# Kernel optimization log

Measured on AMD Instinct MI355X. Metric: run time of the kernel, lower is better.

Reference implementation:

```python
import jax, jax.numpy as jnp
import numpy as np

VOCAB, EMBED, HIDDEN, POL = 32000, 300, 1024, 3
BS, SEQ = 64, 512


def setup_inputs() -> dict:
    key = jax.random.key(0)
    ks = jax.random.split(key, 17)
    stdv = 1.0 / np.sqrt(HIDDEN)
    u = lambda k, shape: jax.random.uniform(k, shape, jnp.float32, -stdv, stdv)
    return {
        "text": jax.random.randint(ks[0], (BS, SEQ), 0, VOCAB),
        "embed_table": jax.random.normal(ks[1], (VOCAB, EMBED), jnp.float32),
        "U_i": u(ks[2], (EMBED, HIDDEN)), "U_f": u(ks[3], (EMBED, HIDDEN)),
        "U_c": u(ks[4], (EMBED, HIDDEN)), "U_o": u(ks[5], (EMBED, HIDDEN)),
        "V_i": u(ks[6], (HIDDEN, HIDDEN)), "V_f": u(ks[7], (HIDDEN, HIDDEN)),
        "V_c": u(ks[8], (HIDDEN, HIDDEN)), "V_o": u(ks[9], (HIDDEN, HIDDEN)),
        "b_i": u(ks[10], (HIDDEN,)), "b_f": u(ks[11], (HIDDEN,)),
        "b_c": u(ks[12], (HIDDEN,)), "b_o": u(ks[13], (HIDDEN,)),
        "W_dense": u(ks[14], (HIDDEN, POL)),
        "b_dense": u(ks[15], (POL,)),
    }


def _lstm_final_h(x, U_i, U_f, U_c, U_o, V_i, V_f, V_c, V_o, b_i, b_f, b_c, b_o):
    # x: [B, S, E]. Precompute all input projections once (big fused GEMM),
    # leaving only the recurrent h @ V matmuls inside the scan.
    bs = x.shape[0]
    H = V_i.shape[0]
    U = jnp.concatenate([U_i, U_f, U_c, U_o], axis=1)          # [E, 4H]
    b = jnp.concatenate([b_i, b_f, b_c, b_o], axis=0)          # [4H]
    xU = jnp.einsum('bse,eh->sbh', x, U) + b                   # [S, B, 4H]
    V = jnp.concatenate([V_i, V_f, V_c, V_o], axis=1)          # [H, 4H]

    def step(carry, xu_t):
        h, c = carry
        gates = xu_t + h @ V                                   # [B, 4H]
        xi, xf, xg, xo = jnp.split(gates, 4, axis=-1)
        i = jax.nn.sigmoid(xi)
        f = jax.nn.sigmoid(xf)
        g = jnp.tanh(xg)
        o = jax.nn.sigmoid(xo)
        c = f * c + i * g
        h = o * jnp.tanh(c)
        return (h, c), None

    h0 = jnp.zeros((bs, H), x.dtype)
    c0 = jnp.zeros((bs, H), x.dtype)
    (h_n, c_n), _ = jax.lax.scan(step, (h0, c0), xU)
    return h_n


def reference(text, embed_table, U_i, U_f, U_c, U_o, V_i, V_f, V_c, V_o,
              b_i, b_f, b_c, b_o, W_dense, b_dense):
    x = embed_table[text]                                      # [B, S, E]
    h_n = _lstm_final_h(x, U_i, U_f, U_c, U_o, V_i, V_f, V_c, V_o,
                        b_i, b_f, b_c, b_o)                    # [B, H]
    return h_n @ W_dense + b_dense                             # [B, POL]
```

## Files before the change

kernel.cpp:

```cpp
#include <hip/hip_runtime.h>
#include <stdint.h>

#define SEQL 512
#define BATCH 64
#define EMB 300
#define EMBP 320
#define HID 1024
#define NWG 64
#define UNITS 16
#define NCH 42
#define FSTR 16

typedef __attribute__((ext_vector_type(8))) short short8;
typedef __attribute__((ext_vector_type(4))) float f32x4;
typedef __attribute__((ext_vector_type(2))) unsigned int uint2v;

union Frag { short8 v; ushort u[8]; uint uu[4]; };
struct AF { uint2v lo, hi; };

__device__ __forceinline__ ushort f2bf(float f){
  union { float f; uint u; } c; c.f = f;
  return (ushort)((c.u + 0x7fffu + ((c.u >> 16) & 1u)) >> 16);
}

struct Params {
  const ushort* xbf;
  ushort* hbuf;
  float*  hfinal;
  int*    flags;
  ushort* wpack;
  const float* V[4];
  const float* U[4];
  const float* bia[4];
  const float* Wd;
  const float* bd;
  float* out;
};

__global__ void __launch_bounds__(256) prep(const int* __restrict__ text,
                                            const float* __restrict__ tab,
                                            ushort* __restrict__ xbf,
                                            ushort* __restrict__ hbuf,
                                            int* __restrict__ flags){
  const int tid = blockIdx.x * blockDim.x + threadIdx.x;
  const int nth = gridDim.x * blockDim.x;
  uint* hz = (uint*)hbuf;
  for (int i = tid; i < NWG*64*16/2; i += nth) hz[i] = 0u;
  if (tid < NWG*FSTR) flags[tid] = 0;
  const int nch = SEQL*BATCH*(EMBP/8);
  for (int ch = tid; ch < nch; ch += nth){
    const int e8 = ch % (EMBP/8);
    const int sb = ch / (EMBP/8);
    const int b  = sb & (BATCH-1);
    const int s  = sb >> 6;
    const int tok = text[b*SEQL + s];
    union { ushort u[8]; uint4 v; } o;
    #pragma unroll
    for (int j = 0; j < 8; j++){
      const int e = e8*8 + j;
      o.u[j] = f2bf(e < EMB ? tab[(size_t)tok*EMB + e] : 0.f);
    }
    *(uint4*)&xbf[(size_t)sb*EMBP + e8*8] = o.v;
  }
}

__global__ void __launch_bounds__(256) packw(Params p){
  const int bid  = blockIdx.x;
  const int w    = bid / NCH;
  const int kc   = bid % NCH;
  const int tid  = threadIdx.x;
  const int nt   = tid >> 6;
  const int lane = tid & 63;
  const int l4   = (lane >> 4) & 3;
  const int colg = w*UNITS + (lane & 15);
  Frag fr;
  #pragma unroll
  for (int j = 0; j < 8; j++){
    const int koff = ((j >> 2) << 4) + l4*4 + (j & 3);
    float v = 0.f;
    if (kc < 32){
      v = p.V[nt][(size_t)(kc*32 + koff)*HID + colg];
    } else {
      const int krow = (kc-32)*32 + koff;
      if (krow < EMB) v = p.U[nt][(size_t)krow*HID + colg];
    }
    fr.u[j] = f2bf(v);
  }
  *(short8*)&p.wpack[(((size_t)(w*NCH + kc)*4 + nt)*64 + lane)*8] = fr.v;
}

#define WISSUE(c) { \
    const ushort* wp_ = wpk + (size_t)(wave + 4*(c))*2048 + lane*8; \
    asm volatile("global_load_dwordx4 %0, %4, off\n\t" \
                 "global_load_dwordx4 %1, %4, off offset:1024\n\t" \
                 "global_load_dwordx4 %2, %4, off offset:2048\n\t" \
                 "global_load_dwordx4 %3, %4, off offset:3072" \
                 : "=&v"(wfr[(c)&3][0]), "=&v"(wfr[(c)&3][1]), \
                   "=&v"(wfr[(c)&3][2]), "=&v"(wfr[(c)&3][3]) \
                 : "v"(wp_) : "memory"); }

#define VISSUE(c) { \
    const ushort* bp_ = hcur + (size_t)(wave + 4*(c))*2048 + qk; \
    _Pragma("unroll") \
    for (int m_ = 0; m_ < 4; m_++){ \
      const ushort* rp_ = bp_ + (m_*16 + mrow)*16; \
      asm volatile("global_load_dwordx2 %0, %2, off sc0 sc1\n\t" \
                   "global_load_dwordx2 %1, %2, off offset:2048 sc0 sc1" \
                   : "=&v"(afr[(c)&3][m_].lo), "=&v"(afr[(c)&3][m_].hi) \
                   : "v"(rp_) : "memory"); \
    } }

#define VWAIT(n) { asm volatile("s_waitcnt vmcnt(" #n ")" ::: "memory"); \
                   __builtin_amdgcn_sched_barrier(0); }

#define VMFMA(c) { \
    _Pragma("unroll") \
    for (int m_ = 0; m_ < 4; m_++){ \
      Frag a_; \
      a_.uu[0] = afr[(c)&3][m_].lo[0]; a_.uu[1] = afr[(c)&3][m_].lo[1]; \
      a_.uu[2] = afr[(c)&3][m_].hi[0]; a_.uu[3] = afr[(c)&3][m_].hi[1]; \
      _Pragma("unroll") \
      for (int nt_ = 0; nt_ < 4; nt_++) \
        acc[m_][nt_] = __builtin_amdgcn_mfma_f32_16x16x32_bf16(a_.v, wfr[(c)&3][nt_], acc[m_][nt_], 0, 0, 0); \
    } }

__global__ void __launch_bounds__(256, 1) lstm_scan(Params p){
  __shared__ float buffer[2][64][68];
  __shared__ float cst[UNITS][BATCH];
  __shared__ float bias_l[64];

  const int w    = blockIdx.x;
  const int tid  = threadIdx.x;
  const int wave = tid >> 6;
  const int lane = tid & 63;
  const int n0   = w * UNITS;
  const int mrow = lane & 15;
  const int qk   = ((lane >> 4) & 3) << 2;
  const int nU   = (wave < 2) ? 3 : 2;
  const ushort* __restrict__ wpk = p.wpack + (size_t)w*NCH*2048;

  const int pl   = lane & 15;
  const int* fp  = p.flags + (2*(wave + 4*(pl >> 1)) + (pl & 1)) * FSTR;

  if (tid < 64) bias_l[tid] = p.bia[tid >> 4][n0 + (tid & 15)];
  for (int i = tid; i < UNITS*BATCH; i += 256) (&cst[0][0])[i] = 0.f;
  __syncthreads();

  for (int t = 0; t < SEQL; t++){
    const ushort* __restrict__ xt = p.xbf + (size_t)t * (BATCH*EMBP);

    f32x4 acc[4][4];
    #pragma unroll
    for (int m = 0; m < 4; m++)
      #pragma unroll
      for (int nt = 0; nt < 4; nt++)
        acc[m][nt] = (f32x4){0.f, 0.f, 0.f, 0.f};

    #pragma unroll
    for (int j3 = 0; j3 < 3; j3++){
      if (j3 < nU){
        const int kb  = (wave + 4*j3)*32;
        const int kcg = 32 + wave + 4*j3;
        Frag af[4];
        #pragma unroll
        for (int m = 0; m < 4; m++){
          const ushort* rp = xt + (size_t)(m*16 + mrow)*EMBP + kb + qk;
          uint2 lo = *(const uint2*)rp;
          uint2 hi = *(const uint2*)(rp + 16);
          af[m].uu[0] = lo.x; af[m].uu[1] = lo.y;
          af[m].uu[2] = hi.x; af[m].uu[3] = hi.y;
        }
        short8 wu[4];
        #pragma unroll
        for (int nt = 0; nt < 4; nt++)
          wu[nt] = *(const short8*)&wpk[(size_t)kcg*2048 + nt*512 + lane*8];
        #pragma unroll
        for (int m = 0; m < 4; m++)
          #pragma unroll
          for (int nt = 0; nt < 4; nt++)
            acc[m][nt] = __builtin_amdgcn_mfma_f32_16x16x32_bf16(af[m].v, wu[nt], acc[m][nt], 0, 0, 0);
      }
    }

    if (t > 0){
      for (;;){
        int v;
        asm volatile("global_load_dword %0, %1, off sc0 sc1\n\t"
                     "s_waitcnt vmcnt(0)"
                     : "=&v"(v) : "v"(fp) : "memory");
        if (__all(v >= t)) break;
        __builtin_amdgcn_s_sleep(1);
      }
      __builtin_amdgcn_sched_barrier(0);

      const ushort* __restrict__ hcur = p.hbuf + (size_t)(t & 1) * (NWG*64*16);
      AF afr[4][4];
      short8 wfr[4][4];
      VWAIT(0)
      WISSUE(0) VISSUE(0) WISSUE(1) VISSUE(1)
      WISSUE(2) VISSUE(2) WISSUE(3) VISSUE(3)
      VWAIT(36) VMFMA(0) WISSUE(4) VISSUE(4)
      VWAIT(36) VMFMA(1) WISSUE(5) VISSUE(5)
      VWAIT(36) VMFMA(2) WISSUE(6) VISSUE(6)
      VWAIT(36) VMFMA(3) WISSUE(7) VISSUE(7)
      VWAIT(36) VMFMA(4)
      VWAIT(24) VMFMA(5)
      VWAIT(12) VMFMA(6)
      VWAIT(0)  VMFMA(7)
    }

    const int fq = (lane >> 4) << 2;
    if (wave >= 2){
      #pragma unroll
      for (int m = 0; m < 4; m++)
        #pragma unroll
        for (int nt = 0; nt < 4; nt++)
          *(f32x4*)&buffer[wave-2][nt*16 + mrow][m*16 + fq] = acc[m][nt];
    }
    __syncthreads();
    if (wave < 2){
      #pragma unroll
      for (int m = 0; m < 4; m++)
        #pragma unroll
        for (int nt = 0; nt < 4; nt++){
          f32x4 o = *(f32x4*)&buffer[wave][nt*16 + mrow][m*16 + fq];
          o += acc[m][nt];
          *(f32x4*)&buffer[wave][nt*16 + mrow][m*16 + fq] = o;
        }
    }
    __syncthreads();

    const int eb = tid & 63;
    const int uq = tid >> 6;
    ushort* __restrict__ hnxt = p.hbuf + (size_t)((t+1) & 1) * (NWG*64*16);
    ushort hout[4]; float hfv[4];
    #pragma unroll
    for (int rr = 0; rr < 4; rr++){
      const int u = uq*4 + rr;
      float g0 = buffer[0][ 0+u][eb] + buffer[1][ 0+u][eb] + bias_l[ 0+u];
      float g1 = buffer[0][16+u][eb] + buffer[1][16+u][eb] + bias_l[16+u];
      float g2 = buffer[0][32+u][eb] + buffer[1][32+u][eb] + bias_l[32+u];
      float g3 = buffer[0][48+u][eb] + buffer[1][48+u][eb] + bias_l[48+u];
      float ig = 1.f/(1.f + __expf(-g0));
      float fg = 1.f/(1.f + __expf(-g1));
      float gg = 2.f/(1.f + __expf(-2.f*g2)) - 1.f;
      float og = 1.f/(1.f + __expf(-g3));
      float cv = fg * cst[u][eb] + ig * gg;
      cst[u][eb] = cv;
      float hv = og * (2.f/(1.f + __expf(-2.f*cv)) - 1.f);
      hout[rr] = f2bf(hv);
      hfv[rr] = hv;
    }
    {
      union { ushort u[4]; uint2v v; } pk;
      pk.u[0]=hout[0]; pk.u[1]=hout[1]; pk.u[2]=hout[2]; pk.u[3]=hout[3];
      ushort* sa = &hnxt[(size_t)w*1024 + eb*16 + uq*4];
      asm volatile("global_store_dwordx2 %0, %1, off sc0 sc1"
                   :: "v"(sa), "v"(pk.v) : "memory");
      if (t == SEQL-1){
        f32x4 fv; fv[0]=hfv[0]; fv[1]=hfv[1]; fv[2]=hfv[2]; fv[3]=hfv[3];
        float* fa = &p.hfinal[(size_t)eb*HID + n0 + uq*4];
        asm volatile("global_store_dwordx4 %0, %1, off sc0 sc1"
                     :: "v"(fa), "v"(fv) : "memory");
      }
    }
    asm volatile("s_waitcnt vmcnt(0)" ::: "memory");
    __syncthreads();
    if (tid == 0){
      int tv = t + 1;
      asm volatile("global_store_dword %0, %1, off sc0 sc1"
                   :: "v"(p.flags + w*FSTR), "v"(tv) : "memory");
    }
  }

  if (wave == 0){
    const int* ffp = p.flags + lane*FSTR;
    for (;;){
      int v;
      asm volatile("global_load_dword %0, %1, off sc0 sc1\n\t"
                   "s_waitcnt vmcnt(0)"
                   : "=&v"(v) : "v"(ffp) : "memory");
      if (__all(v >= SEQL)) break;
      __builtin_amdgcn_s_sleep(1);
    }
  }
  __syncthreads();

  float s0 = 0.f, s1 = 0.f, s2 = 0.f;
  {
    const float* ap = p.hfinal + (size_t)w * HID + tid;
    float h0, h1, h2, h3;
    asm volatile("global_load_dword %0, %4, off sc0 sc1\n\t"
                 "global_load_dword %1, %4, off offset:1024 sc0 sc1\n\t"
                 "global_load_dword %2, %4, off offset:2048 sc0 sc1\n\t"
                 "global_load_dword %3, %4, off offset:3072 sc0 sc1\n\t"
                 "s_waitcnt vmcnt(0)"
                 : "=&v"(h0), "=&v"(h1), "=&v"(h2), "=&v"(h3)
                 : "v"(ap) : "memory");
    const float hvv[4] = {h0, h1, h2, h3};
    #pragma unroll
    for (int j = 0; j < 4; j++){
      const int k = tid + 256*j;
      s0 = fmaf(hvv[j], p.Wd[k*3+0], s0);
      s1 = fmaf(hvv[j], p.Wd[k*3+1], s1);
      s2 = fmaf(hvv[j], p.Wd[k*3+2], s2);
    }
  }
  float* red = &buffer[0][0][0];
  red[tid*3+0] = s0; red[tid*3+1] = s1; red[tid*3+2] = s2;
  __syncthreads();
  for (int off = 128; off > 0; off >>= 1){
    if (tid < off){
      red[tid*3+0] += red[(tid+off)*3+0];
      red[tid*3+1] += red[(tid+off)*3+1];
      red[tid*3+2] += red[(tid+off)*3+2];
    }
    __syncthreads();
  }
  if (tid < 3) p.out[w*3 + tid] = red[tid] + p.bd[tid];
}

extern "C" void kernel_launch(void* const* d_in, const int* in_sizes, int n_in,
                              void* d_out, int out_size, void* d_ws, size_t ws_size,
                              hipStream_t stream){
  const int*   text = (const int*)d_in[0];
  const float* tab  = (const float*)d_in[1];

  Params p;
  char* ws = (char*)d_ws;
  size_t off = 0;
  p.xbf    = (const ushort*)(ws + off); off += (size_t)SEQL*BATCH*EMBP*2;
  p.hbuf   = (ushort*)(ws + off);       off += (size_t)2*NWG*64*16*2;
  p.hfinal = (float*)(ws + off);        off += (size_t)BATCH*HID*4;
  p.flags  = (int*)(ws + off);          off += (size_t)NWG*FSTR*4;
  p.wpack  = (ushort*)(ws + off);       off += (size_t)NWG*NCH*4*64*8*2;

  for (int g = 0; g < 4; g++){
    p.U[g]   = (const float*)d_in[2+g];
    p.V[g]   = (const float*)d_in[6+g];
    p.bia[g] = (const float*)d_in[10+g];
  }
  p.Wd  = (const float*)d_in[14];
  p.bd  = (const float*)d_in[15];
  p.out = (float*)d_out;

  prep<<<1024, 256, 0, stream>>>(text, tab, (ushort*)p.xbf, (ushort*)p.hbuf, p.flags);
  packw<<<NWG*NCH, 256, 0, stream>>>(p);
  lstm_scan<<<NWG, 256, 0, stream>>>(p);
}
```

Before: 4.167 ms.

## Halve persistent workgroups to 32 with 512 threads and gate-split waves

The persistent LSTM scan moves from 64 workgroups of 256 threads with 16 hidden units each to 32 workgroups of 512 threads with 32 units each. Each wave now owns one gate and half of the K range, and the waves are reduced through shared memory. The weight pack layout, h buffer layout, flag polling and final dense reduction are rewritten to match, and the recurrent load pipeline is deepened to 5 stages. The aim is fewer cross-workgroup flag syncs per step and more per-workgroup work to hide latency, at the cost of heavier per-workgroup weight streaming and fewer CUs in use.

```diff
diff --git a/kernel.cpp b/kernel.cpp
--- a/kernel.cpp
+++ b/kernel.cpp
@@ -6,8 +6,8 @@
 #define EMB 300
 #define EMBP 320
 #define HID 1024
-#define NWG 64
-#define UNITS 16
+#define NWG 32
+#define UNITS 32
 #define NCH 42
 #define FSTR 16
 
@@ -45,7 +45,7 @@
   const int tid = blockIdx.x * blockDim.x + threadIdx.x;
   const int nth = gridDim.x * blockDim.x;
   uint* hz = (uint*)hbuf;
-  for (int i = tid; i < NWG*64*16/2; i += nth) hz[i] = 0u;
+  for (int i = tid; i < NWG*64*UNITS/2; i += nth) hz[i] = 0u;
   if (tid < NWG*FSTR) flags[tid] = 0;
   const int nch = SEQL*BATCH*(EMBP/8);
   for (int ch = tid; ch < nch; ch += nth){
@@ -65,48 +65,50 @@
 }
 
 __global__ void __launch_bounds__(256) packw(Params p){
-  const int bid  = blockIdx.x;
-  const int w    = bid / NCH;
-  const int kc   = bid % NCH;
-  const int tid  = threadIdx.x;
-  const int nt   = tid >> 6;
-  const int lane = tid & 63;
-  const int l4   = (lane >> 4) & 3;
-  const int colg = w*UNITS + (lane & 15);
-  Frag fr;
+  const int bid = blockIdx.x;
+  const int w   = bid / NCH;
+  const int kc  = bid % NCH;
+  const int tid = threadIdx.x;
   #pragma unroll
-  for (int j = 0; j < 8; j++){
-    const int koff = ((j >> 2) << 4) + l4*4 + (j & 3);
-    float v = 0.f;
-    if (kc < 32){
-      v = p.V[nt][(size_t)(kc*32 + koff)*HID + colg];
-    } else {
-      const int krow = (kc-32)*32 + koff;
-      if (krow < EMB) v = p.U[nt][(size_t)krow*HID + colg];
-    }
-    fr.u[j] = f2bf(v);
-  }
-  *(short8*)&p.wpack[(((size_t)(w*NCH + kc)*4 + nt)*64 + lane)*8] = fr.v;
+  for (int r = 0; r < 2; r++){
+    const int item = tid + 256*r;
+    const int g    = item >> 7;
+    const int nt   = (item >> 6) & 1;
+    const int lane = item & 63;
+    const int l4   = (lane >> 4) & 3;
+    const int colg = w*UNITS + nt*16 + (lane & 15);
+    Frag fr;
+    #pragma unroll
+    for (int j = 0; j < 8; j++){
+      const int koff = ((j >> 2) << 4) + l4*4 + (j & 3);
+      float v = 0.f;
+      if (kc < 32){
+        v = p.V[g][(size_t)(kc*32 + koff)*HID + colg];
+      } else {
+        const int krow = (kc-32)*32 + koff;
+        if (krow < EMB) v = p.U[g][(size_t)krow*HID + colg];
+      }
+      fr.u[j] = f2bf(v);
+    }
+    *(short8*)&p.wpack[((((size_t)(w*NCH + kc)*4 + g)*2 + nt)*64 + lane)*8] = fr.v;
+  }
 }
 
 #define WISSUE(c) { \
-    const ushort* wp_ = wpk + (size_t)(wave + 4*(c))*2048 + lane*8; \
-    asm volatile("global_load_dwordx4 %0, %4, off\n\t" \
-                 "global_load_dwordx4 %1, %4, off offset:1024\n\t" \
-                 "global_load_dwordx4 %2, %4, off offset:2048\n\t" \
-                 "global_load_dwordx4 %3, %4, off offset:3072" \
-                 : "=&v"(wfr[(c)&3][0]), "=&v"(wfr[(c)&3][1]), \
-                   "=&v"(wfr[(c)&3][2]), "=&v"(wfr[(c)&3][3]) \
+    const ushort* wp_ = wpk + ((size_t)(kh2*16 + (c))*8 + g*2)*512 + lane*8; \
+    asm volatile("global_load_dwordx4 %0, %2, off\n\t" \
+                 "global_load_dwordx4 %1, %2, off offset:1024" \
+                 : "=&v"(wfr[(c)%5][0]), "=&v"(wfr[(c)%5][1]) \
                  : "v"(wp_) : "memory"); }
 
 #define VISSUE(c) { \
-    const ushort* bp_ = hcur + (size_t)(wave + 4*(c))*2048 + qk; \
+    const ushort* bp_ = hcur + (size_t)(kh2*16 + (c))*2048 + qk; \
     _Pragma("unroll") \
     for (int m_ = 0; m_ < 4; m_++){ \
-      const ushort* rp_ = bp_ + (m_*16 + mrow)*16; \
+      const ushort* rp_ = bp_ + (m_*16 + mrow)*32; \
       asm volatile("global_load_dwordx2 %0, %2, off sc0 sc1\n\t" \
-                   "global_load_dwordx2 %1, %2, off offset:2048 sc0 sc1" \
-                   : "=&v"(afr[(c)&3][m_].lo), "=&v"(afr[(c)&3][m_].hi) \
+                   "global_load_dwordx2 %1, %2, off offset:32 sc0 sc1" \
+                   : "=&v"(afr[(c)%5][m_].lo), "=&v"(afr[(c)%5][m_].hi) \
                    : "v"(rp_) : "memory"); \
     } }
 
@@ -117,68 +119,65 @@
     _Pragma("unroll") \
     for (int m_ = 0; m_ < 4; m_++){ \
       Frag a_; \
-      a_.uu[0] = afr[(c)&3][m_].lo[0]; a_.uu[1] = afr[(c)&3][m_].lo[1]; \
-      a_.uu[2] = afr[(c)&3][m_].hi[0]; a_.uu[3] = afr[(c)&3][m_].hi[1]; \
-      _Pragma("unroll") \
-      for (int nt_ = 0; nt_ < 4; nt_++) \
-        acc[m_][nt_] = __builtin_amdgcn_mfma_f32_16x16x32_bf16(a_.v, wfr[(c)&3][nt_], acc[m_][nt_], 0, 0, 0); \
+      a_.uu[0] = afr[(c)%5][m_].lo[0]; a_.uu[1] = afr[(c)%5][m_].lo[1]; \
+      a_.uu[2] = afr[(c)%5][m_].hi[0]; a_.uu[3] = afr[(c)%5][m_].hi[1]; \
+      acc[m_][0] = __builtin_amdgcn_mfma_f32_16x16x32_bf16(a_.v, wfr[(c)%5][0], acc[m_][0], 0, 0, 0); \
+      acc[m_][1] = __builtin_amdgcn_mfma_f32_16x16x32_bf16(a_.v, wfr[(c)%5][1], acc[m_][1], 0, 0, 0); \
     } }
 
-__global__ void __launch_bounds__(256, 1) lstm_scan(Params p){
-  __shared__ float buffer[2][64][68];
+#define STEP5(c) { VWAIT(40) VMFMA(c) WISSUE((c)+5) VISSUE((c)+5) }
+
+__global__ void __launch_bounds__(512, 1) lstm_scan(Params p){
+  __shared__ float buffer[4][UNITS][66];
   __shared__ float cst[UNITS][BATCH];
-  __shared__ float bias_l[64];
+  __shared__ float bias_l[4*UNITS];
 
   const int w    = blockIdx.x;
   const int tid  = threadIdx.x;
   const int wave = tid >> 6;
+  const int g    = wave & 3;
+  const int kh2  = wave >> 2;
   const int lane = tid & 63;
   const int n0   = w * UNITS;
   const int mrow = lane & 15;
   const int qk   = ((lane >> 4) & 3) << 2;
-  const int nU   = (wave < 2) ? 3 : 2;
-  const ushort* __restrict__ wpk = p.wpack + (size_t)w*NCH*2048;
+  const int fq   = (lane >> 4) << 2;
+  const ushort* __restrict__ wpk = p.wpack + (size_t)w*NCH*4096;
 
   const int pl   = lane & 15;
-  const int* fp  = p.flags + (2*(wave + 4*(pl >> 1)) + (pl & 1)) * FSTR;
-
-  if (tid < 64) bias_l[tid] = p.bia[tid >> 4][n0 + (tid & 15)];
-  for (int i = tid; i < UNITS*BATCH; i += 256) (&cst[0][0])[i] = 0.f;
+  const int* fp  = p.flags + (kh2*16 + pl) * FSTR;
+
+  if (tid < 4*UNITS) bias_l[tid] = p.bia[tid >> 5][n0 + (tid & 31)];
+  for (int i = tid; i < UNITS*BATCH; i += 512) (&cst[0][0])[i] = 0.f;
   __syncthreads();
 
   for (int t = 0; t < SEQL; t++){
     const ushort* __restrict__ xt = p.xbf + (size_t)t * (BATCH*EMBP);
 
-    f32x4 acc[4][4];
-    #pragma unroll
-    for (int m = 0; m < 4; m++)
+    f32x4 acc[4][2];
+    #pragma unroll
+    for (int m = 0; m < 4; m++){ acc[m][0] = (f32x4){0,0,0,0}; acc[m][1] = (f32x4){0,0,0,0}; }
+
+    #pragma unroll
+    for (int uc = 0; uc < 5; uc++){
+      const int ug  = kh2*5 + uc;
+      const int kb  = ug*32;
+      const int kcg = 32 + ug;
+      Frag af[4];
       #pragma unroll
-      for (int nt = 0; nt < 4; nt++)
-        acc[m][nt] = (f32x4){0.f, 0.f, 0.f, 0.f};
-
-    #pragma unroll
-    for (int j3 = 0; j3 < 3; j3++){
-      if (j3 < nU){
-        const int kb  = (wave + 4*j3)*32;
-        const int kcg = 32 + wave + 4*j3;
-        Frag af[4];
-        #pragma unroll
-        for (int m = 0; m < 4; m++){
-          const ushort* rp = xt + (size_t)(m*16 + mrow)*EMBP + kb + qk;
-          uint2 lo = *(const uint2*)rp;
-          uint2 hi = *(const uint2*)(rp + 16);
-          af[m].uu[0] = lo.x; af[m].uu[1] = lo.y;
-          af[m].uu[2] = hi.x; af[m].uu[3] = hi.y;
-        }
-        short8 wu[4];
-        #pragma unroll
-        for (int nt = 0; nt < 4; nt++)
-          wu[nt] = *(const short8*)&wpk[(size_t)kcg*2048 + nt*512 + lane*8];
-        #pragma unroll
-        for (int m = 0; m < 4; m++)
-          #pragma unroll
-          for (int nt = 0; nt < 4; nt++)
-            acc[m][nt] = __builtin_amdgcn_mfma_f32_16x16x32_bf16(af[m].v, wu[nt], acc[m][nt], 0, 0, 0);
+      for (int m = 0; m < 4; m++){
+        const ushort* rp = xt + (size_t)(m*16 + mrow)*EMBP + kb + qk;
+        uint2 lo = *(const uint2*)rp;
+        uint2 hi = *(const uint2*)(rp + 16);
+        af[m].uu[0] = lo.x; af[m].uu[1] = lo.y;
+        af[m].uu[2] = hi.x; af[m].uu[3] = hi.y;
+      }
+      short8 wu0 = *(const short8*)&wpk[((size_t)kcg*8 + g*2)*512 + lane*8];
+      short8 wu1 = *(const short8*)&wpk[((size_t)kcg*8 + g*2 + 1)*512 + lane*8];
+      #pragma unroll
+      for (int m = 0; m < 4; m++){
+        acc[m][0] = __builtin_amdgcn_mfma_f32_16x16x32_bf16(af[m].v, wu0, acc[m][0], 0, 0, 0);
+        acc[m][1] = __builtin_amdgcn_mfma_f32_16x16x32_bf16(af[m].v, wu1, acc[m][1], 0, 0, 0);
       }
     }
 
@@ -193,54 +192,53 @@
       }
       __builtin_amdgcn_sched_barrier(0);
 
-      const ushort* __restrict__ hcur = p.hbuf + (size_t)(t & 1) * (NWG*64*16);
-      AF afr[4][4];
-      short8 wfr[4][4];
+      const ushort* __restrict__ hcur = p.hbuf + (size_t)(t & 1) * (NWG*64*UNITS);
+      AF afr[5][4];
+      short8 wfr[5][2];
       VWAIT(0)
-      WISSUE(0) VISSUE(0) WISSUE(1) VISSUE(1)
-      WISSUE(2) VISSUE(2) WISSUE(3) VISSUE(3)
-      VWAIT(36) VMFMA(0) WISSUE(4) VISSUE(4)
-      VWAIT(36) VMFMA(1) WISSUE(5) VISSUE(5)
-      VWAIT(36) VMFMA(2) WISSUE(6) VISSUE(6)
-      VWAIT(36) VMFMA(3) WISSUE(7) VISSUE(7)
-      VWAIT(36) VMFMA(4)
-      VWAIT(24) VMFMA(5)
-      VWAIT(12) VMFMA(6)
-      VWAIT(0)  VMFMA(7)
-    }
-
-    const int fq = (lane >> 4) << 2;
-    if (wave >= 2){
+      WISSUE(0) VISSUE(0) WISSUE(1) VISSUE(1) WISSUE(2) VISSUE(2)
+      WISSUE(3) VISSUE(3) WISSUE(4) VISSUE(4)
+      STEP5(0)  STEP5(1)  STEP5(2)  STEP5(3)
+      STEP5(4)  STEP5(5)  STEP5(6)  STEP5(7)
+      STEP5(8)  STEP5(9)  STEP5(10)
+      VWAIT(40) VMFMA(11)
+      VWAIT(30) VMFMA(12)
+      VWAIT(20) VMFMA(13)
+      VWAIT(10) VMFMA(14)
+      VWAIT(0)  VMFMA(15)
+    }
+
+    if (kh2 == 1){
       #pragma unroll
       for (int m = 0; m < 4; m++)
         #pragma unroll
-        for (int nt = 0; nt < 4; nt++)
-          *(f32x4*)&buffer[wave-2][nt*16 + mrow][m*16 + fq] = acc[m][nt];
+        for (int nt = 0; nt < 2; nt++)
+          *(f32x4*)&buffer[g][nt*16 + mrow][m*16 + fq] = acc[m][nt];
     }
     __syncthreads();
-    if (wave < 2){
+    if (kh2 == 0){
       #pragma unroll
       for (int m = 0; m < 4; m++)
         #pragma unroll
-        for (int nt = 0; nt < 4; nt++){
-          f32x4 o = *(f32x4*)&buffer[wave][nt*16 + mrow][m*16 + fq];
+        for (int nt = 0; nt < 2; nt++){
+          f32x4 o = *(f32x4*)&buffer[g][nt*16 + mrow][m*16 + fq];
           o += acc[m][nt];
-          *(f32x4*)&buffer[wave][nt*16 + mrow][m*16 + fq] = o;
+          *(f32x4*)&buffer[g][nt*16 + mrow][m*16 + fq] = o;
         }
     }
     __syncthreads();
 
     const int eb = tid & 63;
     const int uq = tid >> 6;
-    ushort* __restrict__ hnxt = p.hbuf + (size_t)((t+1) & 1) * (NWG*64*16);
+    ushort* __restrict__ hnxt = p.hbuf + (size_t)((t+1) & 1) * (NWG*64*UNITS);
     ushort hout[4]; float hfv[4];
     #pragma unroll
     for (int rr = 0; rr < 4; rr++){
       const int u = uq*4 + rr;
-      float g0 = buffer[0][ 0+u][eb] + buffer[1][ 0+u][eb] + bias_l[ 0+u];
-      float g1 = buffer[0][16+u][eb] + buffer[1][16+u][eb] + bias_l[16+u];
-      float g2 = buffer[0][32+u][eb] + buffer[1][32+u][eb] + bias_l[32+u];
-      float g3 = buffer[0][48+u][eb] + buffer[1][48+u][eb] + bias_l[48+u];
+      float g0 = buffer[0][u][eb] + bias_l[ 0 + u];
+      float g1 = buffer[1][u][eb] + bias_l[32 + u];
+      float g2 = buffer[2][u][eb] + bias_l[64 + u];
+      float g3 = buffer[3][u][eb] + bias_l[96 + u];
       float ig = 1.f/(1.f + __expf(-g0));
       float fg = 1.f/(1.f + __expf(-g1));
       float gg = 2.f/(1.f + __expf(-2.f*g2)) - 1.f;
@@ -254,7 +252,7 @@
     {
       union { ushort u[4]; uint2v v; } pk;
       pk.u[0]=hout[0]; pk.u[1]=hout[1]; pk.u[2]=hout[2]; pk.u[3]=hout[3];
-      ushort* sa = &hnxt[(size_t)w*1024 + eb*16 + uq*4];
+      ushort* sa = &hnxt[(size_t)w*2048 + eb*32 + uq*4];
       asm volatile("global_store_dwordx2 %0, %1, off sc0 sc1"
                    :: "v"(sa), "v"(pk.v) : "memory");
       if (t == SEQL-1){
@@ -274,7 +272,7 @@
   }
 
   if (wave == 0){
-    const int* ffp = p.flags + lane*FSTR;
+    const int* ffp = p.flags + (lane & 31)*FSTR;
     for (;;){
       int v;
       asm volatile("global_load_dword %0, %1, off sc0 sc1\n\t"
@@ -286,9 +284,12 @@
   }
   __syncthreads();
 
+  const int half  = tid >> 8;
+  const int kbase = tid & 255;
+  const int brow  = 2*w + half;
   float s0 = 0.f, s1 = 0.f, s2 = 0.f;
   {
-    const float* ap = p.hfinal + (size_t)w * HID + tid;
+    const float* ap = p.hfinal + (size_t)brow*HID + kbase;
     float h0, h1, h2, h3;
     asm volatile("global_load_dword %0, %4, off sc0 sc1\n\t"
                  "global_load_dword %1, %4, off offset:1024 sc0 sc1\n\t"
@@ -300,24 +301,27 @@
     const float hvv[4] = {h0, h1, h2, h3};
     #pragma unroll
     for (int j = 0; j < 4; j++){
-      const int k = tid + 256*j;
+      const int k = kbase + 256*j;
       s0 = fmaf(hvv[j], p.Wd[k*3+0], s0);
       s1 = fmaf(hvv[j], p.Wd[k*3+1], s1);
       s2 = fmaf(hvv[j], p.Wd[k*3+2], s2);
     }
   }
   float* red = &buffer[0][0][0];
-  red[tid*3+0] = s0; red[tid*3+1] = s1; red[tid*3+2] = s2;
+  red[(half*256 + kbase)*3 + 0] = s0;
+  red[(half*256 + kbase)*3 + 1] = s1;
+  red[(half*256 + kbase)*3 + 2] = s2;
   __syncthreads();
   for (int off = 128; off > 0; off >>= 1){
-    if (tid < off){
-      red[tid*3+0] += red[(tid+off)*3+0];
-      red[tid*3+1] += red[(tid+off)*3+1];
-      red[tid*3+2] += red[(tid+off)*3+2];
+    if (kbase < off){
+      const int a = (half*256 + kbase)*3, b = (half*256 + kbase + off)*3;
+      red[a+0] += red[b+0];
+      red[a+1] += red[b+1];
+      red[a+2] += red[b+2];
     }
     __syncthreads();
   }
-  if (tid < 3) p.out[w*3 + tid] = red[tid] + p.bd[tid];
+  if (kbase < 3) p.out[brow*3 + kbase] = red[half*256*3 + kbase] + p.bd[kbase];
 }
 
 extern "C" void kernel_launch(void* const* d_in, const int* in_sizes, int n_in,
@@ -330,10 +334,10 @@
   char* ws = (char*)d_ws;
   size_t off = 0;
   p.xbf    = (const ushort*)(ws + off); off += (size_t)SEQL*BATCH*EMBP*2;
-  p.hbuf   = (ushort*)(ws + off);       off += (size_t)2*NWG*64*16*2;
+  p.hbuf   = (ushort*)(ws + off);       off += (size_t)2*NWG*64*UNITS*2;
   p.hfinal = (float*)(ws + off);        off += (size_t)BATCH*HID*4;
   p.flags  = (int*)(ws + off);          off += (size_t)NWG*FSTR*4;
-  p.wpack  = (ushort*)(ws + off);       off += (size_t)NWG*NCH*4*64*8*2;
+  p.wpack  = (ushort*)(ws + off);       off += (size_t)NWG*NCH*4096*2;
 
   for (int g = 0; g < 4; g++){
     p.U[g]   = (const float*)d_in[2+g];
@@ -346,5 +350,5 @@
 
   prep<<<1024, 256, 0, stream>>>(text, tab, (ushort*)p.xbf, (ushort*)p.hbuf, p.flags);
   packw<<<NWG*NCH, 256, 0, stream>>>(p);
-  lstm_scan<<<NWG, 256, 0, stream>>>(p);
-}
+  lstm_scan<<<NWG, 512, 0, stream>>>(p);
+}
```

New measurement: 14.58 ms. 250% more time.
